# Optimization experiments

Hardware: AMD Instinct MI355X
Metric: run time of the kernel (lower is better)

## Reference

```python
import jax, jax.numpy as jnp
import numpy as np

B, S, E, H = 4, 4096, 1024, 16
D = E // H  # head_dim = 64
EPS = 1e-6


def setup_inputs() -> dict:
    key = jax.random.key(0)
    ks = jax.random.split(key, 11)
    inv = 1.0 / np.sqrt(E)
    return {
        "query": jax.random.normal(ks[0], (B, S, E), dtype=jnp.float32),
        "key": jax.random.normal(ks[1], (B, S, E), dtype=jnp.float32),
        "value": jax.random.normal(ks[2], (B, S, E), dtype=jnp.float32),
        "key_padding_mask": jnp.zeros((B, S), dtype=bool),
        "Wq": jax.random.uniform(ks[3], (E, E), jnp.float32, -inv, inv),
        "bq": jnp.zeros((E,), jnp.float32),
        "Wk": jax.random.uniform(ks[4], (E, E), jnp.float32, -inv, inv),
        "bk": jnp.zeros((E,), jnp.float32),
        "Wv": jax.random.uniform(ks[5], (E, E), jnp.float32, -inv, inv),
        "bv": jnp.zeros((E,), jnp.float32),
        "Wo": jax.random.uniform(ks[6], (E, E), jnp.float32, -inv, inv),
        "bo": jnp.zeros((E,), jnp.float32),
    }


def _heads(x):
    # (B,S,E) -> (B,H,S,D)
    return x.reshape(B, -1, H, D).transpose(0, 2, 1, 3)


def reference(query, key, value, key_padding_mask, Wq, bq, Wk, bk, Wv, bv, Wo, bo):
    q = _heads(query @ Wq.T + bq)
    k = _heads(key @ Wk.T + bk)
    v = _heads(value @ Wv.T + bv)

    q_aug = jax.nn.relu(q) + EPS
    k_aug = jax.nn.relu(k) + EPS
    # mask out padded keys: (B,S_k) -> (B,1,S_k,1)
    k_aug = jnp.where(key_padding_mask[:, None, :, None], 0.0, k_aug)

    kv_context = jnp.einsum("bhsd,bhsv->bhdv", k_aug, v)  # (B,H,D,D)
    k_sum = k_aug.sum(axis=2)                                # (B,H,D)
    denom = jnp.einsum("bhqd,bhd->bhq", q_aug, k_sum)
    denom = jnp.maximum(denom, EPS)

    attn = jnp.einsum("bhqd,bhdv->bhqv", q_aug, kv_context) / denom[..., None]
    attn = attn.transpose(0, 2, 1, 3).reshape(B, -1, E)      # (B,S_q,E)
    # dropout is identity in eval mode
    return attn @ Wo.T + bo
```

## Files before the change

### kernel.cpp

```cpp
#include <hip/hip_runtime.h>
#include <hip/hip_bf16.h>
#include <stdint.h>

#define B_ 4
#define S_ 4096
#define E_ 1024
#define H_ 16
#define D_ 64
#define M_ (B_*S_)
constexpr float kEPS = 1e-6f;

typedef unsigned short u16;
typedef unsigned char  u8;
typedef __bf16 bf16x8 __attribute__((ext_vector_type(8)));
typedef float  f32x4  __attribute__((ext_vector_type(4)));
typedef u16    u16x8  __attribute__((ext_vector_type(8)));

typedef const __attribute__((address_space(1))) void* gaddr_t;
typedef __attribute__((address_space(3))) void*       laddr_t;

__device__ __forceinline__ u16 f2bf(float f) {
    union { float f; uint32_t u; } v; v.f = f;
    uint32_t u = v.u;
    u += 0x7fffu + ((u >> 16) & 1u);
    return (u16)(u >> 16);
}
__device__ __forceinline__ float bf2f(u16 h) {
    union { uint32_t u; float f; } v; v.u = ((uint32_t)h) << 16;
    return v.f;
}

__global__ void cvt_kernel(const float* __restrict__ in, u16* __restrict__ out, int n4) {
    int i = blockIdx.x * blockDim.x + threadIdx.x;
    if (i >= n4) return;
    float4 v = reinterpret_cast<const float4*>(in)[i];
    ushort4 o;
    o.x = f2bf(v.x); o.y = f2bf(v.y); o.z = f2bf(v.z); o.w = f2bf(v.w);
    reinterpret_cast<ushort4*>(out)[i] = o;
}

#define BM 256
#define BN 256
#define BK 32
#define NT (E_/BK)
#define TILE (BM*BK)

template<int EPI>
__global__ __launch_bounds__(512, 2)
void gemm_bt(const u16* __restrict__ A, const u16* __restrict__ Bw,
             const float* __restrict__ bias, const u8* __restrict__ mask,
             float* __restrict__ Cf, u16* __restrict__ Cb)
{
    extern __shared__ u16 lds[];
    u16* Asb = lds;
    u16* Bsb = lds + 3*TILE;

    const int tid  = threadIdx.x;
    const int wid  = tid >> 6, lane = tid & 63;
    const int wr   = wid >> 2, wc = wid & 3;
    const int n0   = blockIdx.x * BN;
    const int m0   = blockIdx.y * BM;
    const int fr   = lane & 15;
    const int cg   = lane >> 4;

    const int s0 = tid, s1 = tid + 512;
    const int row0 = s0 >> 2, c0 = s0 & 3;
    const int row1 = s1 >> 2, c1 = s1 & 3;
    const int cc0 = c0 ^ ((row0 >> 1) & 3);
    const int cc1 = c1 ^ ((row1 >> 1) & 3);
    const u16* a0p = A  + (size_t)(m0 + row0)*E_ + cc0*8;
    const u16* a1p = A  + (size_t)(m0 + row1)*E_ + cc1*8;
    const u16* b0p = Bw + (size_t)(n0 + row0)*E_ + cc0*8;
    const u16* b1p = Bw + (size_t)(n0 + row1)*E_ + cc1*8;

    const int fsw = (fr >> 1) & 3;
    int aoff[8], boff[4];
#pragma unroll
    for (int mf = 0; mf < 8; ++mf)
        aoff[mf] = (wr*128 + mf*16 + fr)*BK + ((cg ^ fsw) * 8);
#pragma unroll
    for (int nf = 0; nf < 4; ++nf)
        boff[nf] = (wc*64 + nf*16 + fr)*BK + ((cg ^ fsw) * 8);

    f32x4 acc[8][4] = {};

    float bias_v[4];
#pragma unroll
    for (int nf = 0; nf < 4; ++nf) bias_v[nf] = bias[n0 + wc*64 + nf*16 + fr];

    auto STG = [&](int t, int sb) {
        const size_t ke = (size_t)t * BK;
        __builtin_amdgcn_global_load_lds((gaddr_t)(a0p + ke), (laddr_t)(Asb + sb*TILE + s0*8), 16, 0, 0);
        __builtin_amdgcn_global_load_lds((gaddr_t)(a1p + ke), (laddr_t)(Asb + sb*TILE + s1*8), 16, 0, 0);
        __builtin_amdgcn_global_load_lds((gaddr_t)(b0p + ke), (laddr_t)(Bsb + sb*TILE + s0*8), 16, 0, 0);
        __builtin_amdgcn_global_load_lds((gaddr_t)(b1p + ke), (laddr_t)(Bsb + sb*TILE + s1*8), 16, 0, 0);
    };

    auto COMPUTE = [&](int cb) {
        const u16* Ab = Asb + cb*TILE;
        const u16* Bb = Bsb + cb*TILE;
        bf16x8 af[8], bfv[4];
#pragma unroll
        for (int nf = 0; nf < 4; ++nf) bfv[nf] = *reinterpret_cast<const bf16x8*>(Bb + boff[nf]);
#pragma unroll
        for (int mf = 0; mf < 8; ++mf) af[mf]  = *reinterpret_cast<const bf16x8*>(Ab + aoff[mf]);
        asm volatile("s_waitcnt lgkmcnt(0)" ::: "memory");
        __builtin_amdgcn_sched_barrier(0);
        __builtin_amdgcn_s_setprio(1);
#pragma unroll
        for (int mf = 0; mf < 8; ++mf)
#pragma unroll
            for (int nf = 0; nf < 4; ++nf)
                acc[mf][nf] = __builtin_amdgcn_mfma_f32_16x16x32_bf16(af[mf], bfv[nf], acc[mf][nf], 0, 0, 0);
        __builtin_amdgcn_s_setprio(0);
    };

#define W4 do { asm volatile("s_waitcnt vmcnt(4)" ::: "memory"); \
                __builtin_amdgcn_s_barrier(); \
                __builtin_amdgcn_sched_barrier(0); } while (0)
#define W0 do { asm volatile("s_waitcnt vmcnt(0)" ::: "memory"); \
                __builtin_amdgcn_s_barrier(); \
                __builtin_amdgcn_sched_barrier(0); } while (0)

    STG(0, 0);
    STG(1, 1);

#pragma unroll 1
    for (int tb = 0; tb < (NT - 2) / 3; ++tb) {
        const int t = tb * 3;
        W4; STG(t + 2, 2); COMPUTE(0);
        W4; STG(t + 3, 0); COMPUTE(1);
        W4; STG(t + 4, 1); COMPUTE(2);
    }
    W4; COMPUTE(0);
    W0; COMPUTE(1);

#pragma unroll
    for (int mf = 0; mf < 8; ++mf) {
#pragma unroll
        for (int nf = 0; nf < 4; ++nf) {
            const int gn = n0 + wc*64 + nf*16 + fr;
#pragma unroll
            for (int r = 0; r < 4; ++r) {
                const int gm = m0 + wr*128 + mf*16 + cg*4 + r;
                float x = acc[mf][nf][r] + bias_v[nf];
                if (EPI == 0) {
                    Cf[(size_t)gm*E_ + gn] = x;
                } else if (EPI == 1) {
                    x = fmaxf(x, 0.f) + kEPS;
                    Cb[(size_t)gm*E_ + gn] = f2bf(x);
                } else if (EPI == 2) {
                    x = fmaxf(x, 0.f) + kEPS;
                    if (mask[gm]) x = 0.f;
                    Cb[(size_t)gm*E_ + gn] = f2bf(x);
                } else {
                    Cb[(size_t)gm*E_ + gn] = f2bf(x);
                }
            }
        }
    }
}
#undef W4
#undef W0

#define SC 128
#define NCHUNK (S_/SC)
__global__ __launch_bounds__(256)
void kv_partial_kernel(const u16* __restrict__ Ka, const u16* __restrict__ Vv,
                       float* __restrict__ kvp, float* __restrict__ ksp)
{
    __shared__ u16   Ks[SC*64];
    __shared__ float Vs[SC*64];
    const int bh = blockIdx.x, b = bh >> 4, h = bh & 15;
    const int s0 = blockIdx.y * SC;
    const int tid = threadIdx.x;

    for (int g = tid; g < SC*8; g += 256) {
        int row = g >> 3, c8 = (g & 7) * 8;
        size_t goff = (size_t)(b*S_ + s0 + row)*E_ + h*64 + c8;
        *reinterpret_cast<uint4*>(Ks + row*64 + c8) = *reinterpret_cast<const uint4*>(Ka + goff);
        bf16x8 vv = *reinterpret_cast<const bf16x8*>(Vv + goff);
        f32x4 f0, f1;
#pragma unroll
        for (int j = 0; j < 4; ++j) { f0[j] = (float)vv[j]; f1[j] = (float)vv[4+j]; }
        *reinterpret_cast<f32x4*>(Vs + row*64 + c8)     = f0;
        *reinterpret_cast<f32x4*>(Vs + row*64 + c8 + 4) = f1;
    }
    __syncthreads();

    const int d  = tid >> 2;
    const int v0 = (tid & 3) * 16;
    float acc[16] = {};
    float ks = 0.f;
#pragma unroll 2
    for (int s = 0; s < SC; ++s) {
        float kval = bf2f(Ks[s*64 + d]);
        ks += kval;
        const float* vr = Vs + s*64 + v0;
        f32x4 a0 = *reinterpret_cast<const f32x4*>(vr);
        f32x4 a1 = *reinterpret_cast<const f32x4*>(vr + 4);
        f32x4 a2 = *reinterpret_cast<const f32x4*>(vr + 8);
        f32x4 a3 = *reinterpret_cast<const f32x4*>(vr + 12);
#pragma unroll
        for (int j = 0; j < 4; ++j) {
            acc[j]    += kval * a0[j];
            acc[4+j]  += kval * a1[j];
            acc[8+j]  += kval * a2[j];
            acc[12+j] += kval * a3[j];
        }
    }
    float* dst = kvp + ((size_t)(blockIdx.y*64 + bh)*4096) + d*64 + v0;
#pragma unroll
    for (int j = 0; j < 16; ++j) dst[j] = acc[j];
    if ((tid & 3) == 0) ksp[(size_t)(blockIdx.y*64 + bh)*64 + d] = ks;
}

__global__ void kv_reduce_kernel(const float* __restrict__ kvp, const float* __restrict__ ksp,
                                 float* __restrict__ kv, float* __restrict__ ksum)
{
    int i = blockIdx.x*256 + threadIdx.x;
    float s = 0.f;
#pragma unroll
    for (int c = 0; c < NCHUNK; ++c) s += kvp[(size_t)c*262144 + i];
    kv[i] = s;
    if (i < 4096) {
        float t = 0.f;
#pragma unroll
        for (int c = 0; c < NCHUNK; ++c) t += ksp[(size_t)c*4096 + i];
        ksum[i] = t;
    }
}

__global__ __launch_bounds__(256)
void attn_kernel(const u16* __restrict__ Qa, const float* __restrict__ kv,
                 const float* __restrict__ ksum, u16* __restrict__ attn)
{
    __shared__ float kvs[64*64];
    __shared__ float kss[64];
    const int bh = blockIdx.x, b = bh >> 4, h = bh & 15;
    const int tid = threadIdx.x;
    for (int i = tid; i < 1024; i += 256)
        reinterpret_cast<float4*>(kvs)[i] = reinterpret_cast<const float4*>(kv + (size_t)bh*4096)[i];
    if (tid < 64) kss[tid] = ksum[(size_t)bh*64 + tid];
    __syncthreads();

    const int r  = tid >> 2;
    const int v0 = (tid & 3) * 16;
    const int s  = blockIdx.y*64 + r;
    const u16* qrow = Qa + (size_t)(b*S_ + s)*E_ + h*64;

    bf16x8 qv[8];
#pragma unroll
    for (int g = 0; g < 8; ++g) qv[g] = reinterpret_cast<const bf16x8*>(qrow)[g];

    float denom = 0.f;
#pragma unroll
    for (int g = 0; g < 8; ++g)
#pragma unroll
        for (int j = 0; j < 8; ++j) denom += (float)qv[g][j] * kss[g*8 + j];
    denom = fmaxf(denom, kEPS);
    const float inv = 1.0f / denom;

    float acc[16] = {};
#pragma unroll
    for (int g = 0; g < 8; ++g) {
#pragma unroll
        for (int j = 0; j < 8; ++j) {
            const int d = g*8 + j;
            const float qd = (float)qv[g][j];
            const float* kr = kvs + d*64 + v0;
            f32x4 a0 = *reinterpret_cast<const f32x4*>(kr);
            f32x4 a1 = *reinterpret_cast<const f32x4*>(kr + 4);
            f32x4 a2 = *reinterpret_cast<const f32x4*>(kr + 8);
            f32x4 a3 = *reinterpret_cast<const f32x4*>(kr + 12);
#pragma unroll
            for (int v = 0; v < 4; ++v) {
                acc[v]    += qd * a0[v];
                acc[4+v]  += qd * a1[v];
                acc[8+v]  += qd * a2[v];
                acc[12+v] += qd * a3[v];
            }
        }
    }
    u16x8 o0, o1;
#pragma unroll
    for (int j = 0; j < 8; ++j) { o0[j] = f2bf(acc[j]*inv); o1[j] = f2bf(acc[8+j]*inv); }
    u16* orow = attn + (size_t)(b*S_ + s)*E_ + h*64 + v0;
    *reinterpret_cast<u16x8*>(orow)     = o0;
    *reinterpret_cast<u16x8*>(orow + 8) = o1;
}

extern "C" void kernel_launch(void* const* d_in, const int* in_sizes, int n_in,
                              void* d_out, int out_size, void* d_ws, size_t ws_size,
                              hipStream_t stream)
{
    const float* query = (const float*)d_in[0];
    const float* key   = (const float*)d_in[1];
    const float* value = (const float*)d_in[2];
    const u8*    mask  = (const u8*)d_in[3];
    const float* Wq = (const float*)d_in[4];
    const float* bq = (const float*)d_in[5];
    const float* Wk = (const float*)d_in[6];
    const float* bk = (const float*)d_in[7];
    const float* Wv = (const float*)d_in[8];
    const float* bv = (const float*)d_in[9];
    const float* Wo = (const float*)d_in[10];
    const float* bo = (const float*)d_in[11];
    float* out = (float*)d_out;

    const size_t SZ_ME = (size_t)M_ * E_;
    const size_t SZ_EE = (size_t)E_ * E_;

    char* ws = (char*)d_ws;
    u16* qx  = (u16*)ws; ws += SZ_ME*2;
    u16* kx  = (u16*)ws; ws += SZ_ME*2;
    u16* vx  = (u16*)ws; ws += SZ_ME*2;
    u16* Qa  = (u16*)ws; ws += SZ_ME*2;
    u16* Ka  = (u16*)ws; ws += SZ_ME*2;
    u16* Vv  = (u16*)ws; ws += SZ_ME*2;
    u16* wqb = (u16*)ws; ws += SZ_EE*2;
    u16* wkb = (u16*)ws; ws += SZ_EE*2;
    u16* wvb = (u16*)ws; ws += SZ_EE*2;
    u16* wob = (u16*)ws; ws += SZ_EE*2;

    float* kvp  = (float*)kx;
    float* ksp  = (float*)vx;
    float* kv   = (float*)vx + (size_t)NCHUNK*4096;
    float* ksum = kv + 262144;
    u16*   attn = qx;

    cvt_kernel<<<(int)(SZ_ME/4/256), 256, 0, stream>>>(query, qx, (int)(SZ_ME/4));
    cvt_kernel<<<(int)(SZ_ME/4/256), 256, 0, stream>>>(key,   kx, (int)(SZ_ME/4));
    cvt_kernel<<<(int)(SZ_ME/4/256), 256, 0, stream>>>(value, vx, (int)(SZ_ME/4));
    cvt_kernel<<<(int)(SZ_EE/4/256), 256, 0, stream>>>(Wq, wqb, (int)(SZ_EE/4));
    cvt_kernel<<<(int)(SZ_EE/4/256), 256, 0, stream>>>(Wk, wkb, (int)(SZ_EE/4));
    cvt_kernel<<<(int)(SZ_EE/4/256), 256, 0, stream>>>(Wv, wvb, (int)(SZ_EE/4));
    cvt_kernel<<<(int)(SZ_EE/4/256), 256, 0, stream>>>(Wo, wob, (int)(SZ_EE/4));

    dim3 ggrid(E_/BN, M_/BM);
    constexpr size_t LDS_BYTES = 6 * TILE * sizeof(u16);
    gemm_bt<1><<<ggrid, 512, LDS_BYTES, stream>>>(qx, wqb, bq, nullptr, nullptr, Qa);
    gemm_bt<2><<<ggrid, 512, LDS_BYTES, stream>>>(kx, wkb, bk, mask,    nullptr, Ka);
    gemm_bt<3><<<ggrid, 512, LDS_BYTES, stream>>>(vx, wvb, bv, nullptr, nullptr, Vv);

    kv_partial_kernel<<<dim3(B_*H_, NCHUNK), 256, 0, stream>>>(Ka, Vv, kvp, ksp);
    kv_reduce_kernel<<<1024, 256, 0, stream>>>(kvp, ksp, kv, ksum);

    attn_kernel<<<dim3(B_*H_, S_/64), 256, 0, stream>>>(Qa, kv, ksum, attn);

    gemm_bt<0><<<ggrid, 512, LDS_BYTES, stream>>>(attn, wob, bo, nullptr, out, nullptr);
}
```

Before: 324.3 us.

## Fuse fp32 activation conversion into projection GEMMs and move attention to MFMA

The projection GEMMs now read fp32 activations straight into registers and convert them to bf16 before writing LDS, which removes three large conversion kernels and their bf16 round trips through memory. The KV partial kernel keeps V in bf16 with padded LDS rows and uses a 4x4 outer-product register tiling. The reduce kernel writes a transposed bf16 KV matrix, and the attention kernel computes Q·KV with MFMA over 256-row tiles. The GEMM grid order is also swapped. These changes add register pressure and lower KV precision to bf16 in exchange for less memory traffic and fewer launches.

Measured after the change: 337.1 us. 1.04x slower.

```diff
diff --git a/kernel.cpp b/kernel.cpp
--- a/kernel.cpp
+++ b/kernel.cpp
@@ -29,6 +29,18 @@
     union { uint32_t u; float f; } v; v.u = ((uint32_t)h) << 16;
     return v.f;
 }
+__device__ __forceinline__ float hi2f(uint32_t d) {
+    union { uint32_t u; float f; } v; v.u = d & 0xffff0000u;
+    return v.f;
+}
+__device__ __forceinline__ float lo2f(uint32_t d) {
+    union { uint32_t u; float f; } v; v.u = d << 16;
+    return v.f;
+}
+
+#define VM_WAIT(n) asm volatile("s_waitcnt vmcnt(" #n ")" ::: "memory")
+#define LG0        asm volatile("s_waitcnt lgkmcnt(0)" ::: "memory")
+#define BAR        do { __builtin_amdgcn_s_barrier(); __builtin_amdgcn_sched_barrier(0); } while (0)
 
 __global__ void cvt_kernel(const float* __restrict__ in, u16* __restrict__ out, int n4) {
     int i = blockIdx.x * blockDim.x + threadIdx.x;
@@ -45,11 +57,13 @@
 #define NT (E_/BK)
 #define TILE (BM*BK)
 
+struct AReg { f32x4 r[4]; };
+
 template<int EPI>
 __global__ __launch_bounds__(512, 2)
-void gemm_bt(const u16* __restrict__ A, const u16* __restrict__ Bw,
-             const float* __restrict__ bias, const u8* __restrict__ mask,
-             float* __restrict__ Cf, u16* __restrict__ Cb)
+void gemm_f32a(const float* __restrict__ Af, const u16* __restrict__ Bw,
+               const float* __restrict__ bias, const u8* __restrict__ mask,
+               u16* __restrict__ Cb)
 {
     extern __shared__ u16 lds[];
     u16* Asb = lds;
@@ -58,20 +72,23 @@
     const int tid  = threadIdx.x;
     const int wid  = tid >> 6, lane = tid & 63;
     const int wr   = wid >> 2, wc = wid & 3;
-    const int n0   = blockIdx.x * BN;
-    const int m0   = blockIdx.y * BM;
+    const int m0   = blockIdx.x * BM;
+    const int n0   = blockIdx.y * BN;
     const int fr   = lane & 15;
     const int cg   = lane >> 4;
 
-    const int s0 = tid, s1 = tid + 512;
-    const int row0 = s0 >> 2, c0 = s0 & 3;
-    const int row1 = s1 >> 2, c1 = s1 & 3;
-    const int cc0 = c0 ^ ((row0 >> 1) & 3);
-    const int cc1 = c1 ^ ((row1 >> 1) & 3);
-    const u16* a0p = A  + (size_t)(m0 + row0)*E_ + cc0*8;
-    const u16* a1p = A  + (size_t)(m0 + row1)*E_ + cc1*8;
-    const u16* b0p = Bw + (size_t)(n0 + row0)*E_ + cc0*8;
-    const u16* b1p = Bw + (size_t)(n0 + row1)*E_ + cc1*8;
+    const int arow  = tid >> 1;
+    const int ahalf = tid & 1;
+    const int afrow = (arow >> 1) & 3;
+    const int aslot0 = (ahalf*2)     ^ afrow;
+    const int aslot1 = (ahalf*2 + 1) ^ afrow;
+    const float* aBase = Af + (size_t)(m0 + arow)*E_ + ahalf*16;
+
+    const int sb0 = tid, sb1 = tid + 512;
+    const int brow0 = sb0 >> 2, bc0 = (sb0 & 3) ^ ((brow0 >> 1) & 3);
+    const int brow1 = sb1 >> 2, bc1 = (sb1 & 3) ^ ((brow1 >> 1) & 3);
+    const u16* b0p = Bw + (size_t)(n0 + brow0)*E_ + bc0*8;
+    const u16* b1p = Bw + (size_t)(n0 + brow1)*E_ + bc1*8;
 
     const int fsw = (fr >> 1) & 3;
     int aoff[8], boff[4];
@@ -88,15 +105,32 @@
 #pragma unroll
     for (int nf = 0; nf < 4; ++nf) bias_v[nf] = bias[n0 + wc*64 + nf*16 + fr];
 
-    auto STG = [&](int t, int sb) {
+    AReg RA, RB;
+
+    auto issueA = [&](AReg& R, int t) {
+        const float* p = aBase + (size_t)t*BK;
+#pragma unroll
+        for (int i = 0; i < 4; ++i) R.r[i] = *reinterpret_cast<const f32x4*>(p + i*4);
+    };
+    auto cvtw = [&](const AReg& R, int buf) {
+        bf16x8 h0, h1;
+#pragma unroll
+        for (int j = 0; j < 4; ++j) {
+            h0[j]   = (__bf16)R.r[0][j];
+            h0[4+j] = (__bf16)R.r[1][j];
+            h1[j]   = (__bf16)R.r[2][j];
+            h1[4+j] = (__bf16)R.r[3][j];
+        }
+        u16* base = Asb + buf*TILE + arow*BK;
+        *reinterpret_cast<bf16x8*>(base + aslot0*8) = h0;
+        *reinterpret_cast<bf16x8*>(base + aslot1*8) = h1;
+    };
+    auto stgB = [&](int t, int buf) {
         const size_t ke = (size_t)t * BK;
-        __builtin_amdgcn_global_load_lds((gaddr_t)(a0p + ke), (laddr_t)(Asb + sb*TILE + s0*8), 16, 0, 0);
-        __builtin_amdgcn_global_load_lds((gaddr_t)(a1p + ke), (laddr_t)(Asb + sb*TILE + s1*8), 16, 0, 0);
-        __builtin_amdgcn_global_load_lds((gaddr_t)(b0p + ke), (laddr_t)(Bsb + sb*TILE + s0*8), 16, 0, 0);
-        __builtin_amdgcn_global_load_lds((gaddr_t)(b1p + ke), (laddr_t)(Bsb + sb*TILE + s1*8), 16, 0, 0);
+        __builtin_amdgcn_global_load_lds((gaddr_t)(b0p + ke), (laddr_t)(Bsb + buf*TILE + sb0*8), 16, 0, 0);
+        __builtin_amdgcn_global_load_lds((gaddr_t)(b1p + ke), (laddr_t)(Bsb + buf*TILE + sb1*8), 16, 0, 0);
     };
-
-    auto COMPUTE = [&](int cb) {
+    auto compute = [&](int cb) {
         const u16* Ab = Asb + cb*TILE;
         const u16* Bb = Bsb + cb*TILE;
         bf16x8 af[8], bfv[4];
@@ -115,25 +149,37 @@
         __builtin_amdgcn_s_setprio(0);
     };
 
-#define W4 do { asm volatile("s_waitcnt vmcnt(4)" ::: "memory"); \
-                __builtin_amdgcn_s_barrier(); \
-                __builtin_amdgcn_sched_barrier(0); } while (0)
-#define W0 do { asm volatile("s_waitcnt vmcnt(0)" ::: "memory"); \
-                __builtin_amdgcn_s_barrier(); \
-                __builtin_amdgcn_sched_barrier(0); } while (0)
-
-    STG(0, 0);
-    STG(1, 1);
+    issueA(RA, 0);
+    issueA(RB, 1);
+    VM_WAIT(4);
+    cvtw(RA, 0);
+    stgB(0, 0);
+    stgB(1, 1);
+    LG0; BAR;
+
+#define GBODY(T, XREG, YREG) do { \
+        issueA(XREG, (T)+2); \
+        VM_WAIT(6); \
+        cvtw(YREG, ((T)+1)%3); \
+        LG0; BAR; \
+        stgB((T)+2, ((T)+2)%3); \
+        compute((T)%3); \
+    } while (0)
 
 #pragma unroll 1
-    for (int tb = 0; tb < (NT - 2) / 3; ++tb) {
-        const int t = tb * 3;
-        W4; STG(t + 2, 2); COMPUTE(0);
-        W4; STG(t + 3, 0); COMPUTE(1);
-        W4; STG(t + 4, 1); COMPUTE(2);
-    }
-    W4; COMPUTE(0);
-    W0; COMPUTE(1);
+    for (int tp = 0; tp < 15; ++tp) {
+        const int t = tp*2;
+        GBODY(t,   RA, RB);
+        GBODY(t+1, RB, RA);
+    }
+    VM_WAIT(2);
+    cvtw(RB, 1);
+    LG0; BAR;
+    compute(0);
+    VM_WAIT(0);
+    BAR;
+    compute(1);
+#undef GBODY
 
 #pragma unroll
     for (int mf = 0; mf < 8; ++mf) {
@@ -144,9 +190,7 @@
             for (int r = 0; r < 4; ++r) {
                 const int gm = m0 + wr*128 + mf*16 + cg*4 + r;
                 float x = acc[mf][nf][r] + bias_v[nf];
-                if (EPI == 0) {
-                    Cf[(size_t)gm*E_ + gn] = x;
-                } else if (EPI == 1) {
+                if (EPI == 1) {
                     x = fmaxf(x, 0.f) + kEPS;
                     Cb[(size_t)gm*E_ + gn] = f2bf(x);
                 } else if (EPI == 2) {
@@ -160,134 +204,290 @@
         }
     }
 }
+
+template<int EPI>
+__global__ __launch_bounds__(512, 2)
+void gemm_bt(const u16* __restrict__ A, const u16* __restrict__ Bw,
+             const float* __restrict__ bias, const u8* __restrict__ mask,
+             float* __restrict__ Cf, u16* __restrict__ Cb)
+{
+    extern __shared__ u16 lds[];
+    u16* Asb = lds;
+    u16* Bsb = lds + 3*TILE;
+
+    const int tid  = threadIdx.x;
+    const int wid  = tid >> 6, lane = tid & 63;
+    const int wr   = wid >> 2, wc = wid & 3;
+    const int m0   = blockIdx.x * BM;
+    const int n0   = blockIdx.y * BN;
+    const int fr   = lane & 15;
+    const int cg   = lane >> 4;
+
+    const int s0 = tid, s1 = tid + 512;
+    const int row0 = s0 >> 2, c0 = s0 & 3;
+    const int row1 = s1 >> 2, c1 = s1 & 3;
+    const int cc0 = c0 ^ ((row0 >> 1) & 3);
+    const int cc1 = c1 ^ ((row1 >> 1) & 3);
+    const u16* a0p = A  + (size_t)(m0 + row0)*E_ + cc0*8;
+    const u16* a1p = A  + (size_t)(m0 + row1)*E_ + cc1*8;
+    const u16* b0p = Bw + (size_t)(n0 + row0)*E_ + cc0*8;
+    const u16* b1p = Bw + (size_t)(n0 + row1)*E_ + cc1*8;
+
+    const int fsw = (fr >> 1) & 3;
+    int aoff[8], boff[4];
+#pragma unroll
+    for (int mf = 0; mf < 8; ++mf)
+        aoff[mf] = (wr*128 + mf*16 + fr)*BK + ((cg ^ fsw) * 8);
+#pragma unroll
+    for (int nf = 0; nf < 4; ++nf)
+        boff[nf] = (wc*64 + nf*16 + fr)*BK + ((cg ^ fsw) * 8);
+
+    f32x4 acc[8][4] = {};
+
+    float bias_v[4];
+#pragma unroll
+    for (int nf = 0; nf < 4; ++nf) bias_v[nf] = bias[n0 + wc*64 + nf*16 + fr];
+
+    auto STG = [&](int t, int sb) {
+        const size_t ke = (size_t)t * BK;
+        __builtin_amdgcn_global_load_lds((gaddr_t)(a0p + ke), (laddr_t)(Asb + sb*TILE + s0*8), 16, 0, 0);
+        __builtin_amdgcn_global_load_lds((gaddr_t)(a1p + ke), (laddr_t)(Asb + sb*TILE + s1*8), 16, 0, 0);
+        __builtin_amdgcn_global_load_lds((gaddr_t)(b0p + ke), (laddr_t)(Bsb + sb*TILE + s0*8), 16, 0, 0);
+        __builtin_amdgcn_global_load_lds((gaddr_t)(b1p + ke), (laddr_t)(Bsb + sb*TILE + s1*8), 16, 0, 0);
+    };
+
+    auto COMPUTE = [&](int cb) {
+        const u16* Ab = Asb + cb*TILE;
+        const u16* Bb = Bsb + cb*TILE;
+        bf16x8 af[8], bfv[4];
+#pragma unroll
+        for (int nf = 0; nf < 4; ++nf) bfv[nf] = *reinterpret_cast<const bf16x8*>(Bb + boff[nf]);
+#pragma unroll
+        for (int mf = 0; mf < 8; ++mf) af[mf]  = *reinterpret_cast<const bf16x8*>(Ab + aoff[mf]);
+        asm volatile("s_waitcnt lgkmcnt(0)" ::: "memory");
+        __builtin_amdgcn_sched_barrier(0);
+        __builtin_amdgcn_s_setprio(1);
+#pragma unroll
+        for (int mf = 0; mf < 8; ++mf)
+#pragma unroll
+            for (int nf = 0; nf < 4; ++nf)
+                acc[mf][nf] = __builtin_amdgcn_mfma_f32_16x16x32_bf16(af[mf], bfv[nf], acc[mf][nf], 0, 0, 0);
+        __builtin_amdgcn_s_setprio(0);
+    };
+
+#define W4 do { asm volatile("s_waitcnt vmcnt(4)" ::: "memory"); \
+                __builtin_amdgcn_s_barrier(); \
+                __builtin_amdgcn_sched_barrier(0); } while (0)
+#define W0 do { asm volatile("s_waitcnt vmcnt(0)" ::: "memory"); \
+                __builtin_amdgcn_s_barrier(); \
+                __builtin_amdgcn_sched_barrier(0); } while (0)
+
+    STG(0, 0);
+    STG(1, 1);
+
+#pragma unroll 1
+    for (int tb = 0; tb < (NT - 2) / 3; ++tb) {
+        const int t = tb * 3;
+        W4; STG(t + 2, 2); COMPUTE(0);
+        W4; STG(t + 3, 0); COMPUTE(1);
+        W4; STG(t + 4, 1); COMPUTE(2);
+    }
+    W4; COMPUTE(0);
+    W0; COMPUTE(1);
 #undef W4
 #undef W0
 
-#define SC 128
-#define NCHUNK (S_/SC)
+#pragma unroll
+    for (int mf = 0; mf < 8; ++mf) {
+#pragma unroll
+        for (int nf = 0; nf < 4; ++nf) {
+            const int gn = n0 + wc*64 + nf*16 + fr;
+#pragma unroll
+            for (int r = 0; r < 4; ++r) {
+                const int gm = m0 + wr*128 + mf*16 + cg*4 + r;
+                float x = acc[mf][nf][r] + bias_v[nf];
+                if (EPI == 0) {
+                    Cf[(size_t)gm*E_ + gn] = x;
+                } else {
+                    Cb[(size_t)gm*E_ + gn] = f2bf(x);
+                }
+            }
+        }
+    }
+}
+
+#define KVS 256
+#define KVCH (S_/KVS)
+#define KPAD 72
 __global__ __launch_bounds__(256)
 void kv_partial_kernel(const u16* __restrict__ Ka, const u16* __restrict__ Vv,
                        float* __restrict__ kvp, float* __restrict__ ksp)
 {
-    __shared__ u16   Ks[SC*64];
-    __shared__ float Vs[SC*64];
+    __shared__ u16 Ks[KVS*KPAD];
+    __shared__ u16 Vs[KVS*KPAD];
     const int bh = blockIdx.x, b = bh >> 4, h = bh & 15;
-    const int s0 = blockIdx.y * SC;
+    const int s0 = blockIdx.y * KVS;
     const int tid = threadIdx.x;
 
-    for (int g = tid; g < SC*8; g += 256) {
+#pragma unroll
+    for (int i = 0; i < 8; ++i) {
+        int g = i*256 + tid;
         int row = g >> 3, c8 = (g & 7) * 8;
         size_t goff = (size_t)(b*S_ + s0 + row)*E_ + h*64 + c8;
-        *reinterpret_cast<uint4*>(Ks + row*64 + c8) = *reinterpret_cast<const uint4*>(Ka + goff);
-        bf16x8 vv = *reinterpret_cast<const bf16x8*>(Vv + goff);
-        f32x4 f0, f1;
-#pragma unroll
-        for (int j = 0; j < 4; ++j) { f0[j] = (float)vv[j]; f1[j] = (float)vv[4+j]; }
-        *reinterpret_cast<f32x4*>(Vs + row*64 + c8)     = f0;
-        *reinterpret_cast<f32x4*>(Vs + row*64 + c8 + 4) = f1;
+        *reinterpret_cast<uint4*>(Ks + row*KPAD + c8) = *reinterpret_cast<const uint4*>(Ka + goff);
+        *reinterpret_cast<uint4*>(Vs + row*KPAD + c8) = *reinterpret_cast<const uint4*>(Vv + goff);
     }
     __syncthreads();
 
-    const int d  = tid >> 2;
-    const int v0 = (tid & 3) * 16;
+    const int dg = tid >> 4;
+    const int vg = tid & 15;
     float acc[16] = {};
-    float ks = 0.f;
-#pragma unroll 2
-    for (int s = 0; s < SC; ++s) {
-        float kval = bf2f(Ks[s*64 + d]);
-        ks += kval;
-        const float* vr = Vs + s*64 + v0;
-        f32x4 a0 = *reinterpret_cast<const f32x4*>(vr);
-        f32x4 a1 = *reinterpret_cast<const f32x4*>(vr + 4);
-        f32x4 a2 = *reinterpret_cast<const f32x4*>(vr + 8);
-        f32x4 a3 = *reinterpret_cast<const f32x4*>(vr + 12);
-#pragma unroll
-        for (int j = 0; j < 4; ++j) {
-            acc[j]    += kval * a0[j];
-            acc[4+j]  += kval * a1[j];
-            acc[8+j]  += kval * a2[j];
-            acc[12+j] += kval * a3[j];
-        }
-    }
-    float* dst = kvp + ((size_t)(blockIdx.y*64 + bh)*4096) + d*64 + v0;
-#pragma unroll
-    for (int j = 0; j < 16; ++j) dst[j] = acc[j];
-    if ((tid & 3) == 0) ksp[(size_t)(blockIdx.y*64 + bh)*64 + d] = ks;
-}
-
-__global__ void kv_reduce_kernel(const float* __restrict__ kvp, const float* __restrict__ ksp,
-                                 float* __restrict__ kv, float* __restrict__ ksum)
+#pragma unroll 4
+    for (int s = 0; s < KVS; ++s) {
+        uint2 ku = *reinterpret_cast<const uint2*>(Ks + s*KPAD + dg*4);
+        uint2 vu = *reinterpret_cast<const uint2*>(Vs + s*KPAD + vg*4);
+        float k0 = lo2f(ku.x), k1 = hi2f(ku.x), k2 = lo2f(ku.y), k3 = hi2f(ku.y);
+        float v0 = lo2f(vu.x), v1 = hi2f(vu.x), v2 = lo2f(vu.y), v3 = hi2f(vu.y);
+        acc[0]  += k0*v0; acc[1]  += k0*v1; acc[2]  += k0*v2; acc[3]  += k0*v3;
+        acc[4]  += k1*v0; acc[5]  += k1*v1; acc[6]  += k1*v2; acc[7]  += k1*v3;
+        acc[8]  += k2*v0; acc[9]  += k2*v1; acc[10] += k2*v2; acc[11] += k2*v3;
+        acc[12] += k3*v0; acc[13] += k3*v1; acc[14] += k3*v2; acc[15] += k3*v3;
+    }
+    float* dst = kvp + ((size_t)blockIdx.y*64 + bh)*4096;
+#pragma unroll
+    for (int i = 0; i < 4; ++i) {
+        f32x4 o; o[0] = acc[i*4+0]; o[1] = acc[i*4+1]; o[2] = acc[i*4+2]; o[3] = acc[i*4+3];
+        *reinterpret_cast<f32x4*>(dst + (dg*4+i)*64 + vg*4) = o;
+    }
+
+    __syncthreads();
+    {
+        const int col = tid & 63, grp = tid >> 6;
+        float s = 0.f;
+#pragma unroll 8
+        for (int r = 0; r < 64; ++r) s += bf2f(Ks[(grp*64 + r)*KPAD + col]);
+        ((float*)Vs)[grp*64 + col] = s;
+    }
+    __syncthreads();
+    if (tid < 64) {
+        const float* sc = (const float*)Vs;
+        float t = sc[tid] + sc[64+tid] + sc[128+tid] + sc[192+tid];
+        ksp[((size_t)blockIdx.y*64 + bh)*64 + tid] = t;
+    }
+}
+
+__global__ __launch_bounds__(256)
+void kv_reduce_kernel(const float* __restrict__ kvp, const float* __restrict__ ksp,
+                      u16* __restrict__ kvT, float* __restrict__ ksum)
 {
-    int i = blockIdx.x*256 + threadIdx.x;
-    float s = 0.f;
-#pragma unroll
-    for (int c = 0; c < NCHUNK; ++c) s += kvp[(size_t)c*262144 + i];
-    kv[i] = s;
-    if (i < 4096) {
+    __shared__ u16 T[64*KPAD];
+    const int bh = blockIdx.x, tid = threadIdx.x;
+#pragma unroll
+    for (int j = 0; j < 16; ++j) {
+        int idx = j*256 + tid;
+        int d = idx >> 6, v = idx & 63;
+        float s = 0.f;
+#pragma unroll
+        for (int c = 0; c < KVCH; ++c) s += kvp[((size_t)c*64 + bh)*4096 + idx];
+        T[v*KPAD + d] = f2bf(s);
+    }
+    if (tid < 64) {
         float t = 0.f;
 #pragma unroll
-        for (int c = 0; c < NCHUNK; ++c) t += ksp[(size_t)c*4096 + i];
-        ksum[i] = t;
+        for (int c = 0; c < KVCH; ++c) t += ksp[((size_t)c*64 + bh)*64 + tid];
+        ksum[bh*64 + tid] = t;
+    }
+    __syncthreads();
+#pragma unroll
+    for (int k = 0; k < 2; ++k) {
+        int g = k*256 + tid;
+        int v = g >> 3, c8 = (g & 7) * 8;
+        uint4 q = *reinterpret_cast<const uint4*>(T + v*KPAD + c8);
+        *reinterpret_cast<uint4*>(kvT + (size_t)bh*4096 + g*8) = q;
     }
 }
 
 __global__ __launch_bounds__(256)
-void attn_kernel(const u16* __restrict__ Qa, const float* __restrict__ kv,
+void attn_kernel(const u16* __restrict__ Qa, const u16* __restrict__ kvT,
                  const float* __restrict__ ksum, u16* __restrict__ attn)
 {
-    __shared__ float kvs[64*64];
+    __shared__ u16  Qs[256*64];
+    __shared__ u16  Ts[64*64];
     __shared__ float kss[64];
+    __shared__ float invd[256];
+
     const int bh = blockIdx.x, b = bh >> 4, h = bh & 15;
+    const int s0 = blockIdx.y * 256;
     const int tid = threadIdx.x;
-    for (int i = tid; i < 1024; i += 256)
-        reinterpret_cast<float4*>(kvs)[i] = reinterpret_cast<const float4*>(kv + (size_t)bh*4096)[i];
-    if (tid < 64) kss[tid] = ksum[(size_t)bh*64 + tid];
+    const int wid = tid >> 6, lane = tid & 63;
+    const int fr = lane & 15, cg = lane >> 4;
+
+#pragma unroll
+    for (int j = 0; j < 8; ++j) {
+        int L = (wid*8 + j)*64 + lane;
+        int row = L >> 3, c = L & 7;
+        int cs = c ^ (row & 7);
+        const u16* src = Qa + (size_t)(b*S_ + s0 + row)*E_ + h*64 + cs*8;
+        __builtin_amdgcn_global_load_lds((gaddr_t)src, (laddr_t)(Qs + L*8), 16, 0, 0);
+    }
+#pragma unroll
+    for (int k = 0; k < 2; ++k) {
+        int g = k*256 + tid;
+        int v = g >> 3, c = g & 7;
+        uint4 q = *reinterpret_cast<const uint4*>(kvT + (size_t)bh*4096 + g*8);
+        int cs = c ^ (v & 7);
+        *reinterpret_cast<uint4*>(Ts + v*64 + cs*8) = q;
+    }
+    if (tid < 64) kss[tid] = ksum[bh*64 + tid];
+    asm volatile("s_waitcnt vmcnt(0) lgkmcnt(0)" ::: "memory");
     __syncthreads();
 
-    const int r  = tid >> 2;
-    const int v0 = (tid & 3) * 16;
-    const int s  = blockIdx.y*64 + r;
-    const u16* qrow = Qa + (size_t)(b*S_ + s)*E_ + h*64;
-
-    bf16x8 qv[8];
-#pragma unroll
-    for (int g = 0; g < 8; ++g) qv[g] = reinterpret_cast<const bf16x8*>(qrow)[g];
-
-    float denom = 0.f;
-#pragma unroll
-    for (int g = 0; g < 8; ++g)
-#pragma unroll
-        for (int j = 0; j < 8; ++j) denom += (float)qv[g][j] * kss[g*8 + j];
-    denom = fmaxf(denom, kEPS);
-    const float inv = 1.0f / denom;
-
-    float acc[16] = {};
-#pragma unroll
-    for (int g = 0; g < 8; ++g) {
-#pragma unroll
-        for (int j = 0; j < 8; ++j) {
-            const int d = g*8 + j;
-            const float qd = (float)qv[g][j];
-            const float* kr = kvs + d*64 + v0;
-            f32x4 a0 = *reinterpret_cast<const f32x4*>(kr);
-            f32x4 a1 = *reinterpret_cast<const f32x4*>(kr + 4);
-            f32x4 a2 = *reinterpret_cast<const f32x4*>(kr + 8);
-            f32x4 a3 = *reinterpret_cast<const f32x4*>(kr + 12);
-#pragma unroll
-            for (int v = 0; v < 4; ++v) {
-                acc[v]    += qd * a0[v];
-                acc[4+v]  += qd * a1[v];
-                acc[8+v]  += qd * a2[v];
-                acc[12+v] += qd * a3[v];
+    {
+        float den = 0.f;
+#pragma unroll
+        for (int c = 0; c < 8; ++c) {
+            uint4 qc = *reinterpret_cast<const uint4*>(Qs + tid*64 + (c ^ (tid & 7))*8);
+            den += lo2f(qc.x)*kss[c*8+0] + hi2f(qc.x)*kss[c*8+1]
+                 + lo2f(qc.y)*kss[c*8+2] + hi2f(qc.y)*kss[c*8+3]
+                 + lo2f(qc.z)*kss[c*8+4] + hi2f(qc.z)*kss[c*8+5]
+                 + lo2f(qc.w)*kss[c*8+6] + hi2f(qc.w)*kss[c*8+7];
+        }
+        invd[tid] = 1.0f / fmaxf(den, kEPS);
+    }
+    __syncthreads();
+
+    f32x4 acc[4][4] = {};
+#pragma unroll
+    for (int ks = 0; ks < 2; ++ks) {
+        bf16x8 bfrag[4];
+#pragma unroll
+        for (int nf = 0; nf < 4; ++nf) {
+            int v = nf*16 + fr;
+            bfrag[nf] = *reinterpret_cast<const bf16x8*>(Ts + v*64 + ((ks*4 + cg) ^ (v & 7))*8);
+        }
+#pragma unroll
+        for (int mf = 0; mf < 4; ++mf) {
+            int m = wid*64 + mf*16 + fr;
+            bf16x8 afrag = *reinterpret_cast<const bf16x8*>(Qs + m*64 + ((ks*4 + cg) ^ (m & 7))*8);
+#pragma unroll
+            for (int nf = 0; nf < 4; ++nf)
+                acc[mf][nf] = __builtin_amdgcn_mfma_f32_16x16x32_bf16(afrag, bfrag[nf], acc[mf][nf], 0, 0, 0);
+        }
+    }
+
+#pragma unroll
+    for (int mf = 0; mf < 4; ++mf) {
+#pragma unroll
+        for (int nf = 0; nf < 4; ++nf) {
+            const int v = nf*16 + fr;
+#pragma unroll
+            for (int r = 0; r < 4; ++r) {
+                const int row = wid*64 + mf*16 + cg*4 + r;
+                float x = acc[mf][nf][r] * invd[row];
+                attn[(size_t)(b*S_ + s0 + row)*E_ + h*64 + v] = f2bf(x);
             }
         }
     }
-    u16x8 o0, o1;
-#pragma unroll
-    for (int j = 0; j < 8; ++j) { o0[j] = f2bf(acc[j]*inv); o1[j] = f2bf(acc[8+j]*inv); }
-    u16* orow = attn + (size_t)(b*S_ + s)*E_ + h*64 + v0;
-    *reinterpret_cast<u16x8*>(orow)     = o0;
-    *reinterpret_cast<u16x8*>(orow + 8) = o1;
 }
 
 extern "C" void kernel_launch(void* const* d_in, const int* in_sizes, int n_in,
@@ -312,41 +512,34 @@
     const size_t SZ_EE = (size_t)E_ * E_;
 
     char* ws = (char*)d_ws;
-    u16* qx  = (u16*)ws; ws += SZ_ME*2;
-    u16* kx  = (u16*)ws; ws += SZ_ME*2;
-    u16* vx  = (u16*)ws; ws += SZ_ME*2;
-    u16* Qa  = (u16*)ws; ws += SZ_ME*2;
-    u16* Ka  = (u16*)ws; ws += SZ_ME*2;
-    u16* Vv  = (u16*)ws; ws += SZ_ME*2;
-    u16* wqb = (u16*)ws; ws += SZ_EE*2;
-    u16* wkb = (u16*)ws; ws += SZ_EE*2;
-    u16* wvb = (u16*)ws; ws += SZ_EE*2;
-    u16* wob = (u16*)ws; ws += SZ_EE*2;
-
-    float* kvp  = (float*)kx;
-    float* ksp  = (float*)vx;
-    float* kv   = (float*)vx + (size_t)NCHUNK*4096;
-    float* ksum = kv + 262144;
-    u16*   attn = qx;
-
-    cvt_kernel<<<(int)(SZ_ME/4/256), 256, 0, stream>>>(query, qx, (int)(SZ_ME/4));
-    cvt_kernel<<<(int)(SZ_ME/4/256), 256, 0, stream>>>(key,   kx, (int)(SZ_ME/4));
-    cvt_kernel<<<(int)(SZ_ME/4/256), 256, 0, stream>>>(value, vx, (int)(SZ_ME/4));
+    u16* Qa   = (u16*)ws; ws += SZ_ME*2;
+    u16* Ka   = (u16*)ws; ws += SZ_ME*2;
+    u16* Vv   = (u16*)ws; ws += SZ_ME*2;
+    u16* attnb= (u16*)ws; ws += SZ_ME*2;
+    u16* wqb  = (u16*)ws; ws += SZ_EE*2;
+    u16* wkb  = (u16*)ws; ws += SZ_EE*2;
+    u16* wvb  = (u16*)ws; ws += SZ_EE*2;
+    u16* wob  = (u16*)ws; ws += SZ_EE*2;
+    float* kvp = (float*)ws; ws += (size_t)KVCH*64*4096*4;
+    float* ksp = (float*)ws; ws += (size_t)KVCH*64*64*4;
+    u16*  kvT  = (u16*)ws;  ws += (size_t)64*4096*2;
+    float* ksum= (float*)ws; ws += 4096*4;
+
     cvt_kernel<<<(int)(SZ_EE/4/256), 256, 0, stream>>>(Wq, wqb, (int)(SZ_EE/4));
     cvt_kernel<<<(int)(SZ_EE/4/256), 256, 0, stream>>>(Wk, wkb, (int)(SZ_EE/4));
     cvt_kernel<<<(int)(SZ_EE/4/256), 256, 0, stream>>>(Wv, wvb, (int)(SZ_EE/4));
     cvt_kernel<<<(int)(SZ_EE/4/256), 256, 0, stream>>>(Wo, wob, (int)(SZ_EE/4));
 
-    dim3 ggrid(E_/BN, M_/BM);
+    dim3 ggrid(M_/BM, E_/BN);
     constexpr size_t LDS_BYTES = 6 * TILE * sizeof(u16);
-    gemm_bt<1><<<ggrid, 512, LDS_BYTES, stream>>>(qx, wqb, bq, nullptr, nullptr, Qa);
-    gemm_bt<2><<<ggrid, 512, LDS_BYTES, stream>>>(kx, wkb, bk, mask,    nullptr, Ka);
-    gemm_bt<3><<<ggrid, 512, LDS_BYTES, stream>>>(vx, wvb, bv, nullptr, nullptr, Vv);
-
-    kv_partial_kernel<<<dim3(B_*H_, NCHUNK), 256, 0, stream>>>(Ka, Vv, kvp, ksp);
-    kv_reduce_kernel<<<1024, 256, 0, stream>>>(kvp, ksp, kv, ksum);
-
-    attn_kernel<<<dim3(B_*H_, S_/64), 256, 0, stream>>>(Qa, kv, ksum, attn);
-
-    gemm_bt<0><<<ggrid, 512, LDS_BYTES, stream>>>(attn, wob, bo, nullptr, out, nullptr);
-}
+    gemm_f32a<1><<<ggrid, 512, LDS_BYTES, stream>>>(query, wqb, bq, nullptr, Qa);
+    gemm_f32a<2><<<ggrid, 512, LDS_BYTES, stream>>>(key,   wkb, bk, mask,    Ka);
+    gemm_f32a<3><<<ggrid, 512, LDS_BYTES, stream>>>(value, wvb, bv, nullptr, Vv);
+
+    kv_partial_kernel<<<dim3(B_*H_, KVCH), 256, 0, stream>>>(Ka, Vv, kvp, ksp);
+    kv_reduce_kernel<<<64, 256, 0, stream>>>(kvp, ksp, kvT, ksum);
+
+    attn_kernel<<<dim3(B_*H_, S_/256), 256, 0, stream>>>(Qa, kvT, ksum, attnb);
+
+    gemm_bt<0><<<ggrid, 512, LDS_BYTES, stream>>>(attnb, wob, bo, nullptr, out, nullptr);
+}
```
